# Optimization experiments

Hardware: AMD Instinct MI355X
Metric: run time of the kernel (lower is better)

## Reference

```python
import jax, jax.numpy as jnp
import numpy as np

VOCAB = 32000; DIM = 512; NL = 6; B = 2; L = 1024
DI = 2 * DIM      # d_inner (expand=2)
DS = 16           # d_state
DC = 4            # d_conv
DR = DIM // 16    # dt_rank = ceil(512/16) = 32


def setup_inputs() -> dict:
    key = jax.random.key(0)
    ks = jax.random.split(key, 10)
    s = 0.02
    tokens = jax.random.randint(ks[0], (B, L), 0, VOCAB)
    pos_emb = jax.random.normal(ks[1], (1, L, DIM)) * s
    embed = jax.random.normal(ks[2], (VOCAB, DIM)) * s
    lm_w = jax.random.normal(ks[3], (VOCAB, DIM)) * s
    lm_b = jnp.zeros((VOCAB,), jnp.float32)
    in_proj_w = jax.random.normal(ks[4], (NL, 2 * DI, DIM)) * s
    conv_w = jax.random.normal(ks[5], (NL, DI, DC)) * s
    conv_b = jnp.zeros((NL, DI), jnp.float32)
    x_proj_w = jax.random.normal(ks[6], (NL, DR + 2 * DS, DI)) * s
    dt_proj_w = jax.random.normal(ks[7], (NL, DI, DR)) * s
    dt_proj_b = jnp.broadcast_to(jnp.log(jnp.expm1(jnp.float32(0.01))), (NL, DI)).astype(jnp.float32)
    A_log = jnp.log(jnp.broadcast_to(jnp.arange(1, DS + 1, dtype=jnp.float32), (NL, DI, DS)))
    Dp = jnp.ones((NL, DI), jnp.float32)
    out_w = jax.random.normal(ks[8], (NL, DIM, DI)) * s
    ln_g = jnp.ones((NL, DIM), jnp.float32)
    ln_b = jnp.zeros((NL, DIM), jnp.float32)
    return dict(tokens=tokens, pos_emb=pos_emb, embed=embed, lm_w=lm_w, lm_b=lm_b,
                in_proj_w=in_proj_w, conv_w=conv_w, conv_b=conv_b, x_proj_w=x_proj_w,
                dt_proj_w=dt_proj_w, dt_proj_b=dt_proj_b, A_log=A_log, Dp=Dp,
                out_w=out_w, ln_g=ln_g, ln_b=ln_b)


def silu(x):
    return x * jax.nn.sigmoid(x)


def layernorm(x, g, b, eps=1e-5):
    mu = jnp.mean(x, -1, keepdims=True)
    var = jnp.var(x, -1, keepdims=True)
    return (x - mu) * jax.lax.rsqrt(var + eps) * g + b


def causal_dwconv(x, w, b):
    # x: (B,L,DI), w: (DI,DC) depthwise, left-pad causal
    xp = jnp.pad(x, ((0, 0), (DC - 1, 0), (0, 0)))
    y = b
    for k in range(DC):
        y = y + w[:, k] * xp[:, k:k + x.shape[1], :]
    return y


def selective_scan(u, dt, A, Bm, Cm, Dp):
    # u,dt: (B,L,DI); A: (DI,DS); Bm,Cm: (B,L,DS)
    dA = jnp.exp(dt[..., None] * A)                       # (B,L,DI,DS)
    dBu = dt[..., None] * Bm[:, :, None, :] * u[..., None]
    h0 = jnp.zeros((u.shape[0], DI, DS), u.dtype)

    def step(h, inp):
        dA_t, dBu_t, C_t = inp
        h = dA_t * h + dBu_t
        y = jnp.einsum('bdn,bn->bd', h, C_t)
        return h, y

    _, ys = jax.lax.scan(step, h0, (dA.transpose(1, 0, 2, 3),
                                    dBu.transpose(1, 0, 2, 3),
                                    Cm.transpose(1, 0, 2)))
    return ys.transpose(1, 0, 2) + u * Dp


def mamba_block(x, in_w, cw, cb, xp_w, dtw, dtb, A_log, Dp, ow):
    xz = jnp.einsum('bld,ed->ble', x, in_w)               # (B,L,2*DI)
    xc, z = jnp.split(xz, 2, axis=-1)
    xc = silu(causal_dwconv(xc, cw, cb))
    x_dbl = jnp.einsum('bld,ed->ble', xc, xp_w)           # (B,L,DR+2*DS)
    dt, Bm, Cm = jnp.split(x_dbl, [DR, DR + DS], axis=-1)
    dt = jax.nn.softplus(jnp.einsum('blr,dr->bld', dt, dtw) + dtb)
    A = -jnp.exp(A_log)
    y = selective_scan(xc, dt, A, Bm, Cm, Dp)
    y = y * silu(z)
    return jnp.einsum('bld,ed->ble', y, ow)


def reference(tokens, pos_emb, embed, lm_w, lm_b, in_proj_w, conv_w, conv_b,
              x_proj_w, dt_proj_w, dt_proj_b, A_log, Dp, out_w, ln_g, ln_b):
    x = embed[tokens] + pos_emb[:, :tokens.shape[1]]
    for i in range(NL):
        res = x
        x = mamba_block(x, in_proj_w[i], conv_w[i], conv_b[i], x_proj_w[i],
                        dt_proj_w[i], dt_proj_b[i], A_log[i], Dp[i], out_w[i])
        x = layernorm(x + res, ln_g[i], ln_b[i])
    return jnp.einsum('bld,vd->blv', x, lm_w) + lm_b
```

## Files before the change

kernel.cpp:

```cpp
#include <hip/hip_runtime.h>
#include <hip/hip_bf16.h>
#include <math.h>

#define BB 2
#define LL 1024
#define DIM 512
#define NL 6
#define DI 1024
#define DS 16
#define DC 4
#define DR 32
#define VOCAB 32000
#define M_ROWS (BB * LL)
#define CCH 64
#define CHLEN (LL / CCH)
#define KSPLIT 8
#define OSPLIT 2

typedef unsigned short u16;
typedef __attribute__((ext_vector_type(8))) short bf16x8;
typedef __attribute__((ext_vector_type(4))) float f32x4;

__device__ __forceinline__ u16 f2bf(float f) {
    unsigned u = __float_as_uint(f);
    u += 0x7FFF + ((u >> 16) & 1);
    return (u16)(u >> 16);
}
__device__ __forceinline__ float bf2f(u16 h) {
    return __uint_as_float(((unsigned)h) << 16);
}
#define SWZ(r, c) ((c) ^ (((r) >> 1) & 3))

__global__ __launch_bounds__(256) void cast_all(const float* __restrict__ lm,
                                                const float* __restrict__ inw,
                                                const float* __restrict__ ow,
                                                const float* __restrict__ xp,
                                                u16* __restrict__ lmb,
                                                u16* __restrict__ inb,
                                                u16* __restrict__ owb_,
                                                u16* __restrict__ xpb) {
    int idx = blockIdx.x * 256 + threadIdx.x;
    const float* src; u16* dst; int off;
    if (idx < 2048000)      { src = lm;  dst = lmb;  off = idx; }
    else if (idx < 2834432) { src = inw; dst = inb;  off = idx - 2048000; }
    else if (idx < 3227648) { src = ow;  dst = owb_; off = idx - 2834432; }
    else                    { src = xp;  dst = xpb;  off = idx - 3227648; }
    float4 v0 = ((const float4*)src)[off * 2];
    float4 v1 = ((const float4*)src)[off * 2 + 1];
    union { u16 h[8]; int4 v; } r;
    r.h[0] = f2bf(v0.x); r.h[1] = f2bf(v0.y); r.h[2] = f2bf(v0.z); r.h[3] = f2bf(v0.w);
    r.h[4] = f2bf(v1.x); r.h[5] = f2bf(v1.y); r.h[6] = f2bf(v1.z); r.h[7] = f2bf(v1.w);
    ((int4*)dst)[off] = r.v;
}

__global__ __launch_bounds__(256) void embed_kernel(const int* __restrict__ tok,
                                                    const float* __restrict__ pos,
                                                    const float* __restrict__ emb,
                                                    float* __restrict__ x,
                                                    u16* __restrict__ xb) {
    int idx = blockIdx.x * 256 + threadIdx.x;
    int d = idx & (DIM - 1);
    int l = (idx >> 9) & (LL - 1);
    int b = idx >> 19;
    int t = tok[b * LL + l];
    float v = emb[(size_t)t * DIM + d] + pos[l * DIM + d];
    x[idx] = v;
    xb[idx] = f2bf(v);
}

__global__ __launch_bounds__(512) void gemm_256(const u16* __restrict__ A,
                                                const u16* __restrict__ W,
                                                float* __restrict__ C,
                                                const float* __restrict__ bias,
                                                int K, int N) {
    __shared__ __align__(16) char smem_raw[98304];
    u16* As = (u16*)smem_raw;
    u16* Ws = (u16*)(smem_raw + 49152);
    float* Cs = (float*)smem_raw;

    const int t = threadIdx.x;
    const int l = t & 63;
    const int w = t >> 6;
    const int wr = w >> 2;
    const int wc = w & 3;

    const int nwg = gridDim.x;
    const int q8 = nwg >> 3, r8 = nwg & 7;
    const int xcd = blockIdx.x & 7, rank = blockIdx.x >> 3;
    const int wgid = (xcd < r8 ? xcd * (q8 + 1) : r8 * (q8 + 1) + (xcd - r8) * q8) + rank;
    const int bm = (wgid & 7) * 256;
    const int bn = (wgid >> 3) * 256;

    f32x4 acc[8][4] = {};
    const int nt = K >> 5;

    auto STAGE = [&](int bufi, int k0) {
#pragma unroll
        for (int p = 0; p < 2; ++p) {
            const int g = p * 512 + t;
            const int row = g >> 2, slot = g & 3;
            __builtin_amdgcn_global_load_lds(
                (const __attribute__((address_space(1))) unsigned int*)
                    (A + (size_t)(bm + row) * K + k0 + SWZ(row, slot) * 8),
                (__attribute__((address_space(3))) unsigned int*)
                    (As + bufi * 8192 + (p * 512 + w * 64) * 8),
                16, 0, 0);
        }
#pragma unroll
        for (int p = 0; p < 2; ++p) {
            const int g = p * 512 + t;
            const int row = g >> 2, slot = g & 3;
            __builtin_amdgcn_global_load_lds(
                (const __attribute__((address_space(1))) unsigned int*)
                    (W + (size_t)(bn + row) * K + k0 + SWZ(row, slot) * 8),
                (__attribute__((address_space(3))) unsigned int*)
                    (Ws + bufi * 8192 + (p * 512 + w * 64) * 8),
                16, 0, 0);
        }
    };
    auto COMPUTE = [&](int bufi) {
        const u16* Ab = As + bufi * 8192;
        const u16* Wb = Ws + bufi * 8192;
        bf16x8 bfr[4];
#pragma unroll
        for (int ni = 0; ni < 4; ++ni) {
            const int wrow = wc * 64 + ni * 16 + (l & 15);
            bfr[ni] = *(const bf16x8*)(Wb + wrow * 32 + SWZ(wrow, l >> 4) * 8);
        }
        __builtin_amdgcn_s_setprio(1);
#pragma unroll
        for (int mi = 0; mi < 8; ++mi) {
            const int arow = wr * 128 + mi * 16 + (l & 15);
            bf16x8 a = *(const bf16x8*)(Ab + arow * 32 + SWZ(arow, l >> 4) * 8);
#pragma unroll
            for (int ni = 0; ni < 4; ++ni)
                acc[mi][ni] = __builtin_amdgcn_mfma_f32_16x16x32_bf16(bfr[ni], a, acc[mi][ni], 0, 0, 0);
        }
        __builtin_amdgcn_s_setprio(0);
    };

    STAGE(0, 0);
    STAGE(1, 32);
    int b0 = 0;
    for (int tt = 0; tt < nt - 2; ++tt) {
        int b2 = b0 + 2; if (b2 >= 3) b2 -= 3;
        STAGE(b2, (tt + 2) << 5);
        asm volatile("s_waitcnt vmcnt(8)\ns_barrier" ::: "memory");
        COMPUTE(b0);
        asm volatile("s_waitcnt lgkmcnt(0)\ns_barrier" ::: "memory");
        ++b0; if (b0 == 3) b0 = 0;
    }
    asm volatile("s_waitcnt vmcnt(4)\ns_barrier" ::: "memory");
    COMPUTE(b0);
    asm volatile("s_waitcnt lgkmcnt(0)\ns_barrier" ::: "memory");
    ++b0; if (b0 == 3) b0 = 0;
    asm volatile("s_waitcnt vmcnt(0)\ns_barrier" ::: "memory");
    COMPUTE(b0);
    asm volatile("s_waitcnt lgkmcnt(0)" ::: "memory");
    __syncthreads();

#pragma unroll
    for (int pass = 0; pass < 4; ++pass) {
        if (wr == (pass >> 1)) {
            const int pm0 = (pass & 1) * 4;
#pragma unroll
            for (int mi2 = 0; mi2 < 4; ++mi2) {
                const int r = mi2 * 16 + (l & 15);
#pragma unroll
                for (int ni = 0; ni < 4; ++ni) {
                    const int c = wc * 64 + ni * 16 + ((l >> 4) << 2);
                    float4 v;
                    v.x = acc[pm0 + mi2][ni][0]; v.y = acc[pm0 + mi2][ni][1];
                    v.z = acc[pm0 + mi2][ni][2]; v.w = acc[pm0 + mi2][ni][3];
                    *(float4*)(Cs + r * 260 + c) = v;
                }
            }
        }
        __syncthreads();
#pragma unroll
        for (int it = 0; it < 8; ++it) {
            const int idx = it * 512 + t;
            const int r = idx >> 6;
            const int c4 = (idx & 63) * 4;
            float4 v = *(float4*)(Cs + r * 260 + c4);
            if (bias != nullptr) {
                float4 b4 = *(const float4*)(bias + bn + c4);
                v.x += b4.x; v.y += b4.y; v.z += b4.z; v.w += b4.w;
            }
            *(float4*)(C + (size_t)(bm + pass * 64 + r) * N + bn + c4) = v;
        }
        __syncthreads();
    }
}

__global__ __launch_bounds__(256) void gemm_n64(const u16* __restrict__ A,
                                                const u16* __restrict__ W,
                                                float* __restrict__ out,
                                                u16* __restrict__ outb,
                                                const float* __restrict__ bias,
                                                int lda, int ldw, int ldc,
                                                int KS, int pstride) {
    __shared__ __align__(16) char smem_raw[36864];
    u16* As = (u16*)smem_raw;
    u16* Ws = (u16*)(smem_raw + 24576);
    float* Cs = (float*)smem_raw;

    const int t = threadIdx.x;
    const int l = t & 63;
    const int w = t >> 6;
    const int gx = gridDim.x, gy = gridDim.y;
    const int nwg = gx * gy * gridDim.z;
    const int fid = (blockIdx.z * gy + blockIdx.y) * gx + blockIdx.x;
    const int q8 = nwg >> 3, r8 = nwg & 7;
    const int xcd = fid & 7, rank = fid >> 3;
    const int wgid = (xcd < r8 ? xcd * (q8 + 1) : r8 * (q8 + 1) + (xcd - r8) * q8) + rank;
    const int kz = wgid % gx;
    const int bm = ((wgid / gx) % gy) * 128;
    const int bnn = (wgid / (gx * gy)) * 64;
    const int wm = w * 32;

    f32x4 acc[2][4] = {};
    const int nt = KS >> 5;
    const int kbeg = kz * KS;

    auto STAGE = [&](int bufi, int k0) {
#pragma unroll
        for (int p = 0; p < 2; ++p) {
            const int i = p * 256 + w * 64 + l;
            const int row = i >> 2;
            const int kq = SWZ(row, i & 3);
            __builtin_amdgcn_global_load_lds(
                (const __attribute__((address_space(1))) unsigned int*)
                    (A + (size_t)(bm + row) * lda + k0 + kq * 8),
                (__attribute__((address_space(3))) unsigned int*)
                    (As + bufi * 4096 + (p * 256 + w * 64) * 8),
                16, 0, 0);
        }
        {
            const int i = w * 64 + l;
            const int row = i >> 2;
            const int kq = SWZ(row, i & 3);
            __builtin_amdgcn_global_load_lds(
                (const __attribute__((address_space(1))) unsigned int*)
                    (W + (size_t)(bnn + row) * ldw + k0 + kq * 8),
                (__attribute__((address_space(3))) unsigned int*)
                    (Ws + bufi * 2048 + (w * 64) * 8),
                16, 0, 0);
        }
    };
    auto COMPUTE = [&](int bufi) {
        const u16* Ab = As + bufi * 4096;
        const u16* Wb = Ws + bufi * 2048;
        bf16x8 bfr[4];
#pragma unroll
        for (int ni = 0; ni < 4; ++ni) {
            const int wr2 = ni * 16 + (l & 15);
            bfr[ni] = *(const bf16x8*)(Wb + wr2 * 32 + SWZ(wr2, l >> 4) * 8);
        }
        __builtin_amdgcn_s_setprio(1);
#pragma unroll
        for (int mi = 0; mi < 2; ++mi) {
            const int ar = wm + mi * 16 + (l & 15);
            bf16x8 a = *(const bf16x8*)(Ab + ar * 32 + SWZ(ar, l >> 4) * 8);
#pragma unroll
            for (int ni = 0; ni < 4; ++ni)
                acc[mi][ni] = __builtin_amdgcn_mfma_f32_16x16x32_bf16(bfr[ni], a, acc[mi][ni], 0, 0, 0);
        }
        __builtin_amdgcn_s_setprio(0);
    };

    STAGE(0, kbeg);
    if (nt == 1) {
        asm volatile("s_waitcnt vmcnt(0)\ns_barrier" ::: "memory");
        COMPUTE(0);
        asm volatile("s_waitcnt lgkmcnt(0)" ::: "memory");
    } else {
        STAGE(1, kbeg + 32);
        int b0 = 0;
        for (int tt = 0; tt < nt - 2; ++tt) {
            int b2 = b0 + 2; if (b2 >= 3) b2 -= 3;
            STAGE(b2, kbeg + ((tt + 2) << 5));
            asm volatile("s_waitcnt vmcnt(6)\ns_barrier" ::: "memory");
            COMPUTE(b0);
            asm volatile("s_waitcnt lgkmcnt(0)\ns_barrier" ::: "memory");
            ++b0; if (b0 == 3) b0 = 0;
        }
        asm volatile("s_waitcnt vmcnt(3)\ns_barrier" ::: "memory");
        COMPUTE(b0);
        asm volatile("s_waitcnt lgkmcnt(0)\ns_barrier" ::: "memory");
        ++b0; if (b0 == 3) b0 = 0;
        asm volatile("s_waitcnt vmcnt(0)\ns_barrier" ::: "memory");
        COMPUTE(b0);
        asm volatile("s_waitcnt lgkmcnt(0)" ::: "memory");
    }

    if (outb != nullptr) {
        u16* opb = outb + (size_t)kz * pstride;
#pragma unroll
        for (int mi = 0; mi < 2; ++mi) {
            const int row = bm + wm + mi * 16 + (l & 15);
#pragma unroll
            for (int ni = 0; ni < 4; ++ni) {
                const int col = bnn + ni * 16 + ((l >> 4) << 2);
                ushort4 v;
                v.x = f2bf(acc[mi][ni][0]); v.y = f2bf(acc[mi][ni][1]);
                v.z = f2bf(acc[mi][ni][2]); v.w = f2bf(acc[mi][ni][3]);
                *(ushort4*)(opb + (size_t)row * ldc + col) = v;
            }
        }
    } else {
        float* op = out + (size_t)kz * pstride;
        __syncthreads();
#pragma unroll
        for (int pass = 0; pass < 2; ++pass) {
            if ((w >> 1) == pass) {
                const int rbase = (w & 1) * 32;
#pragma unroll
                for (int mi = 0; mi < 2; ++mi) {
                    const int r = rbase + mi * 16 + (l & 15);
#pragma unroll
                    for (int ni = 0; ni < 4; ++ni) {
                        const int c = ni * 16 + ((l >> 4) << 2);
                        float4 v;
                        v.x = acc[mi][ni][0]; v.y = acc[mi][ni][1];
                        v.z = acc[mi][ni][2]; v.w = acc[mi][ni][3];
                        *(float4*)(Cs + r * 65 + c) = v;
                    }
                }
            }
            __syncthreads();
#pragma unroll
            for (int it = 0; it < 4; ++it) {
                const int idx = it * 256 + t;
                const int r = idx >> 4;
                const int c4 = (idx & 15) * 4;
                float4 v = *(float4*)(Cs + r * 65 + c4);
                if (bias != nullptr) {
                    float4 b4 = *(const float4*)(bias + bnn + c4);
                    v.x += b4.x; v.y += b4.y; v.z += b4.z; v.w += b4.w;
                }
                *(float4*)(op + (size_t)(bm + pass * 64 + r) * ldc + bnn + c4) = v;
            }
            __syncthreads();
        }
    }
}

__global__ __launch_bounds__(256) void conv_silu(const u16* __restrict__ xzb,
                                                 const float* __restrict__ cw,
                                                 const float* __restrict__ cb,
                                                 u16* __restrict__ xcb) {
    int idx8 = blockIdx.x * 256 + threadIdx.x;
    int c0 = (idx8 & 127) * 8;
    int m = idx8 >> 7;
    int l = m & (LL - 1);

    float acc[8];
    float4 cb0 = *(const float4*)(cb + c0);
    float4 cb1 = *(const float4*)(cb + c0 + 4);
    acc[0] = cb0.x; acc[1] = cb0.y; acc[2] = cb0.z; acc[3] = cb0.w;
    acc[4] = cb1.x; acc[5] = cb1.y; acc[6] = cb1.z; acc[7] = cb1.w;
#pragma unroll
    for (int k = 0; k < DC; ++k) {
        int ll = l + k - (DC - 1);
        if (ll < 0) continue;
        const u16* row = xzb + ((size_t)(m + k - (DC - 1))) * (2 * DI) + c0;
        ushort4 r0 = *(const ushort4*)row;
        ushort4 r1 = *(const ushort4*)(row + 4);
#pragma unroll
        for (int j = 0; j < 4; ++j) {
            acc[j]     += cw[(c0 + j) * DC + k]     * bf2f(((const u16*)&r0)[j]);
            acc[j + 4] += cw[(c0 + j + 4) * DC + k] * bf2f(((const u16*)&r1)[j]);
        }
    }
    ushort4 o0, o1;
#pragma unroll
    for (int j = 0; j < 4; ++j) {
        float v0 = acc[j]     / (1.f + __expf(-acc[j]));
        float v1 = acc[j + 4] / (1.f + __expf(-acc[j + 4]));
        ((u16*)&o0)[j] = f2bf(v0);
        ((u16*)&o1)[j] = f2bf(v1);
    }
    u16* op = xcb + (size_t)idx8 * 8;
    *(ushort4*)op = o0;
    *(ushort4*)(op + 4) = o1;
}

__global__ __launch_bounds__(256) void scan_pass1(const u16* __restrict__ xcb,
                                                  const float* __restrict__ Pf,
                                                  const float* __restrict__ dtw,
                                                  const float* __restrict__ dtb,
                                                  const float* __restrict__ A_log,
                                                  float* __restrict__ S,
                                                  float* __restrict__ Q) {
    __shared__ float xds[CHLEN][64];
    const int t = threadIdx.x;
    const int d = blockIdx.x * 256 + t;
    const int b = blockIdx.y;
    const int c = blockIdx.z;
    const int l0 = c * CHLEN;
    const int m0 = b * LL + l0;

    for (int i = t; i < CHLEN * 64; i += 256) {
        int r = i >> 6, cc = i & 63;
        float s = 0.f;
#pragma unroll
        for (int kz = 0; kz < KSPLIT; ++kz)
            s += Pf[(size_t)kz * (M_ROWS * 64) + (m0 + r) * 64 + cc];
        xds[r][cc] = s;
    }
    __syncthreads();

    float4 wreg[8];
#pragma unroll
    for (int kk = 0; kk < 8; ++kk)
        wreg[kk] = *(const float4*)(dtw + (size_t)d * DR + kk * 4);
    const float dtbv = dtb[d];

    float a[DS];
#pragma unroll
    for (int q = 0; q < 4; ++q) {
        float4 al = *(const float4*)(A_log + d * DS + q * 4);
        a[q * 4 + 0] = -__expf(al.x);
        a[q * 4 + 1] = -__expf(al.y);
        a[q * 4 + 2] = -__expf(al.z);
        a[q * 4 + 3] = -__expf(al.w);
    }
    float Qr[DS];
#pragma unroll
    for (int n = 0; n < DS; ++n) Qr[n] = 0.f;
    float Ssum = 0.f;

    const u16* up = xcb + (size_t)m0 * DI + d;

    for (int l = 0; l < CHLEN; ++l) {
        float dacc = dtbv;
#pragma unroll
        for (int kk = 0; kk < 8; ++kk) {
            float4 xv = *(const float4*)&xds[l][kk * 4];
            dacc += wreg[kk].x * xv.x + wreg[kk].y * xv.y +
                    wreg[kk].z * xv.z + wreg[kk].w * xv.w;
        }
        float dtv = (dacc > 20.f) ? dacc : log1pf(__expf(dacc));
        float uv = bf2f(up[(size_t)l * DI]);
        float wv = dtv * uv;
        Ssum += dtv;
#pragma unroll
        for (int q = 0; q < 4; ++q) {
            float4 Bv = *(const float4*)&xds[l][32 + q * 4];
            float dA0 = __expf(dtv * a[q * 4 + 0]);
            float dA1 = __expf(dtv * a[q * 4 + 1]);
            float dA2 = __expf(dtv * a[q * 4 + 2]);
            float dA3 = __expf(dtv * a[q * 4 + 3]);
            Qr[q * 4 + 0] = dA0 * Qr[q * 4 + 0] + wv * Bv.x;
            Qr[q * 4 + 1] = dA1 * Qr[q * 4 + 1] + wv * Bv.y;
            Qr[q * 4 + 2] = dA2 * Qr[q * 4 + 2] + wv * Bv.z;
            Qr[q * 4 + 3] = dA3 * Qr[q * 4 + 3] + wv * Bv.w;
        }
    }
    S[((size_t)b * CCH + c) * DI + d] = Ssum;
    float* Qp = Q + (((size_t)b * CCH + c) * DI + d) * DS;
#pragma unroll
    for (int q = 0; q < 4; ++q) {
        float4 o;
        o.x = Qr[q * 4 + 0]; o.y = Qr[q * 4 + 1];
        o.z = Qr[q * 4 + 2]; o.w = Qr[q * 4 + 3];
        *(float4*)(Qp + q * 4) = o;
    }
}

__global__ __launch_bounds__(64) void scan_pass2(const float* __restrict__ A_log,
                                                 const float* __restrict__ S,
                                                 float* __restrict__ Q) {
    const int idx = blockIdx.x * 64 + threadIdx.x;
    const int b = idx >> 14;
    const int dn = idx & 16383;
    const int d = dn >> 4;
    const float a = -__expf(A_log[dn]);
    float h = 0.f;
    for (int c = 0; c < CCH; ++c) {
        const size_t soff = ((size_t)b * CCH + c) * DI + d;
        const size_t qoff = ((size_t)b * CCH + c) * (size_t)(DI * DS) + dn;
        float P = __expf(a * S[soff]);
        float qv = Q[qoff];
        Q[qoff] = h;
        h = P * h + qv;
    }
}

__global__ __launch_bounds__(256) void scan_pass3(const u16* __restrict__ xcb,
                                                  const float* __restrict__ Pf,
                                                  const float* __restrict__ dtw,
                                                  const float* __restrict__ dtb,
                                                  const u16* __restrict__ xzb,
                                                  const float* __restrict__ A_log,
                                                  const float* __restrict__ Dpp,
                                                  const float* __restrict__ Q,
                                                  u16* __restrict__ y) {
    __shared__ float xds[CHLEN][64];
    const int t = threadIdx.x;
    const int d = blockIdx.x * 256 + t;
    const int b = blockIdx.y;
    const int c = blockIdx.z;
    const int l0 = c * CHLEN;
    const int m0 = b * LL + l0;

    for (int i = t; i < CHLEN * 64; i += 256) {
        int r = i >> 6, cc = i & 63;
        float s = 0.f;
#pragma unroll
        for (int kz = 0; kz < KSPLIT; ++kz)
            s += Pf[(size_t)kz * (M_ROWS * 64) + (m0 + r) * 64 + cc];
        xds[r][cc] = s;
    }
    __syncthreads();

    float4 wreg[8];
#pragma unroll
    for (int kk = 0; kk < 8; ++kk)
        wreg[kk] = *(const float4*)(dtw + (size_t)d * DR + kk * 4);
    const float dtbv = dtb[d];

    float a[DS];
#pragma unroll
    for (int q = 0; q < 4; ++q) {
        float4 al = *(const float4*)(A_log + d * DS + q * 4);
        a[q * 4 + 0] = -__expf(al.x);
        a[q * 4 + 1] = -__expf(al.y);
        a[q * 4 + 2] = -__expf(al.z);
        a[q * 4 + 3] = -__expf(al.w);
    }
    float h[DS];
    const float* Qp = Q + (((size_t)b * CCH + c) * DI + d) * DS;
#pragma unroll
    for (int q = 0; q < 4; ++q) {
        float4 hv = *(const float4*)(Qp + q * 4);
        h[q * 4 + 0] = hv.x; h[q * 4 + 1] = hv.y;
        h[q * 4 + 2] = hv.z; h[q * 4 + 3] = hv.w;
    }
    const float dp = Dpp[d];

    const u16* up = xcb + (size_t)m0 * DI + d;
    const u16* zp = xzb + (size_t)m0 * (2 * DI) + DI + d;
    u16* yp = y + (size_t)m0 * DI + d;

    for (int l = 0; l < CHLEN; ++l) {
        float dacc = dtbv;
#pragma unroll
        for (int kk = 0; kk < 8; ++kk) {
            float4 xv = *(const float4*)&xds[l][kk * 4];
            dacc += wreg[kk].x * xv.x + wreg[kk].y * xv.y +
                    wreg[kk].z * xv.z + wreg[kk].w * xv.w;
        }
        float dtv = (dacc > 20.f) ? dacc : log1pf(__expf(dacc));
        float uv = bf2f(up[(size_t)l * DI]);
        float wv = dtv * uv;
        float p = 0.f;
#pragma unroll
        for (int q = 0; q < 4; ++q) {
            float4 Bv = *(const float4*)&xds[l][32 + q * 4];
            float4 Cv = *(const float4*)&xds[l][48 + q * 4];
            float dA0 = __expf(dtv * a[q * 4 + 0]);
            float dA1 = __expf(dtv * a[q * 4 + 1]);
            float dA2 = __expf(dtv * a[q * 4 + 2]);
            float dA3 = __expf(dtv * a[q * 4 + 3]);
            h[q * 4 + 0] = dA0 * h[q * 4 + 0] + wv * Bv.x;
            h[q * 4 + 1] = dA1 * h[q * 4 + 1] + wv * Bv.y;
            h[q * 4 + 2] = dA2 * h[q * 4 + 2] + wv * Bv.z;
            h[q * 4 + 3] = dA3 * h[q * 4 + 3] + wv * Bv.w;
            p += h[q * 4 + 0] * Cv.x + h[q * 4 + 1] * Cv.y +
                 h[q * 4 + 2] * Cv.z + h[q * 4 + 3] * Cv.w;
        }
        float zv = bf2f(zp[(size_t)l * (2 * DI)]);
        float g = zv / (1.f + __expf(-zv));
        yp[(size_t)l * DI] = f2bf((p + uv * dp) * g);
    }
}

__global__ __launch_bounds__(256) void add_ln(const float* __restrict__ opart,
                                              float* __restrict__ x,
                                              const float* __restrict__ g,
                                              const float* __restrict__ b,
                                              u16* __restrict__ xb) {
    const int PS = M_ROWS * DIM;
    int m = blockIdx.x;
    int t = threadIdx.x;
    const float* xr = x + (size_t)m * DIM;
    float v0 = xr[t];
    float v1 = xr[t + 256];
#pragma unroll
    for (int kz = 0; kz < OSPLIT; ++kz) {
        const float* op = opart + (size_t)kz * PS + (size_t)m * DIM;
        v0 += op[t];
        v1 += op[t + 256];
    }
    float s = v0 + v1;
    float ss = v0 * v0 + v1 * v1;
#pragma unroll
    for (int off = 32; off > 0; off >>= 1) {
        s += __shfl_down(s, off, 64);
        ss += __shfl_down(ss, off, 64);
    }
    __shared__ float sb[4], ssb[4];
    int w = t >> 6;
    if ((t & 63) == 0) { sb[w] = s; ssb[w] = ss; }
    __syncthreads();
    float stot = sb[0] + sb[1] + sb[2] + sb[3];
    float sstot = ssb[0] + ssb[1] + ssb[2] + ssb[3];
    float mean = stot * (1.f / DIM);
    float var = sstot * (1.f / DIM) - mean * mean;
    float rs = rsqrtf(var + 1e-5f);
    float* xw = x + (size_t)m * DIM;
    float o0 = (v0 - mean) * rs * g[t] + b[t];
    float o1 = (v1 - mean) * rs * g[t + 256] + b[t + 256];
    xw[t] = o0;
    xw[t + 256] = o1;
    xb[(size_t)m * DIM + t] = f2bf(o0);
    xb[(size_t)m * DIM + t + 256] = f2bf(o1);
}

extern "C" void kernel_launch(void* const* d_in, const int* in_sizes, int n_in,
                              void* d_out, int out_size, void* d_ws, size_t ws_size,
                              hipStream_t stream) {
    const int*   tokens = (const int*)d_in[0];
    const float* pos    = (const float*)d_in[1];
    const float* emb    = (const float*)d_in[2];
    const float* lm_w   = (const float*)d_in[3];
    const float* lm_b   = (const float*)d_in[4];
    const float* in_w   = (const float*)d_in[5];
    const float* cw     = (const float*)d_in[6];
    const float* cb     = (const float*)d_in[7];
    const float* xpw    = (const float*)d_in[8];
    const float* dtw    = (const float*)d_in[9];
    const float* dtb    = (const float*)d_in[10];
    const float* A_log  = (const float*)d_in[11];
    const float* Dpp    = (const float*)d_in[12];
    const float* ow     = (const float*)d_in[13];
    const float* lng    = (const float*)d_in[14];
    const float* lnb    = (const float*)d_in[15];
    float* out = (float*)d_out;

    float* ws = (float*)d_ws;
    float* x    = ws;
    float* S    = x + 1048576;
    float* Qb   = S + 131072;
    float* Pf   = Qb + 2097152;
    float* Pf2  = Pf + 1048576;
    u16* xzb    = (u16*)(Pf2 + 2097152);
    u16* xb     = xzb + 4194304;
    u16* yb     = xb + 1048576;
    u16* xcb    = yb + 2097152;
    u16* lm_wb  = xcb + 2097152;
    u16* in_wb  = lm_wb + 16384000;
    u16* owb    = in_wb + 6291456;
    u16* xpwb   = owb + 3145728;

    cast_all<<<12800, 256, 0, stream>>>(lm_w, in_w, ow, xpw,
                                        lm_wb, in_wb, owb, xpwb);

    embed_kernel<<<M_ROWS * DIM / 256, 256, 0, stream>>>(tokens, pos, emb, x, xb);

    for (int i = 0; i < NL; ++i) {
        gemm_n64<<<dim3(1, M_ROWS / 128, 2048 / 64), 256, 0, stream>>>(
            xb, in_wb + (size_t)i * 2048 * 512, nullptr, xzb, nullptr,
            512, 512, 2048, 512, 0);
        conv_silu<<<M_ROWS * DI / 8 / 256, 256, 0, stream>>>(
            xzb, cw + (size_t)i * DI * DC, cb + (size_t)i * DI, xcb);
        gemm_n64<<<dim3(KSPLIT, M_ROWS / 128, 1), 256, 0, stream>>>(
            xcb, xpwb + (size_t)i * 64 * 1024, Pf, nullptr, nullptr,
            1024, 1024, 64, 1024 / KSPLIT, M_ROWS * 64);
        scan_pass1<<<dim3(DI / 256, BB, CCH), 256, 0, stream>>>(
            xcb, Pf, dtw + (size_t)i * DI * DR, dtb + (size_t)i * DI,
            A_log + (size_t)i * DI * DS, S, Qb);
        scan_pass2<<<(BB * DI * DS) / 64, 64, 0, stream>>>(
            A_log + (size_t)i * DI * DS, S, Qb);
        scan_pass3<<<dim3(DI / 256, BB, CCH), 256, 0, stream>>>(
            xcb, Pf, dtw + (size_t)i * DI * DR, dtb + (size_t)i * DI, xzb,
            A_log + (size_t)i * DI * DS, Dpp + (size_t)i * DI, Qb, yb);
        gemm_n64<<<dim3(OSPLIT, M_ROWS / 128, 512 / 64), 256, 0, stream>>>(
            yb, owb + (size_t)i * 512 * 1024, Pf2, nullptr, nullptr,
            1024, 1024, 512, 1024 / OSPLIT, M_ROWS * 512);
        add_ln<<<M_ROWS, 256, 0, stream>>>(
            Pf2, x, lng + (size_t)i * DIM, lnb + (size_t)i * DIM, xb);
    }

    gemm_256<<<(M_ROWS / 256) * (VOCAB / 256), 512, 0, stream>>>(
        xb, lm_wb, out, lm_b, 512, VOCAB);
}
```

Baseline: 793.9 us.

## Fuse three scan passes into one cooperative kernel with grid syncs

Merges the chunked selective-scan passes (per-chunk local scan, cross-chunk carry propagation, final output pass) into a single cooperative kernel separated by grid-wide syncs. Each block keeps its dt, A and xds state in registers and shared memory across phases. This removes two kernel launches per layer and the recomputation of the projection reduction and dt weights in the third pass. In exchange it adds grid barrier overhead, requires all 512 blocks to be co-resident, and the carry phase now runs 256-thread blocks in a sequential loop over chunks.

New measurement: 1.671 ms. 2.11x slower.

```diff
diff --git a/kernel.cpp b/kernel.cpp
--- a/kernel.cpp
+++ b/kernel.cpp
@@ -1,6 +1,9 @@
 #include <hip/hip_runtime.h>
 #include <hip/hip_bf16.h>
+#include <hip/hip_cooperative_groups.h>
 #include <math.h>
+
+namespace cg = cooperative_groups;
 
 #define BB 2
 #define LL 1024
@@ -386,13 +389,16 @@
     *(ushort4*)(op + 4) = o1;
 }
 
-__global__ __launch_bounds__(256) void scan_pass1(const u16* __restrict__ xcb,
-                                                  const float* __restrict__ Pf,
-                                                  const float* __restrict__ dtw,
-                                                  const float* __restrict__ dtb,
-                                                  const float* __restrict__ A_log,
-                                                  float* __restrict__ S,
-                                                  float* __restrict__ Q) {
+__global__ __launch_bounds__(256) void scan_coop(const u16* __restrict__ xcb,
+                                                 const float* __restrict__ Pf,
+                                                 const float* __restrict__ dtw,
+                                                 const float* __restrict__ dtb,
+                                                 const u16* __restrict__ xzb,
+                                                 const float* __restrict__ A_log,
+                                                 const float* __restrict__ Dpp,
+                                                 float* S,
+                                                 float* Q,
+                                                 u16* __restrict__ y) {
     __shared__ float xds[CHLEN][64];
     const int t = threadIdx.x;
     const int d = blockIdx.x * 256 + t;
@@ -426,11 +432,11 @@
         a[q * 4 + 2] = -__expf(al.z);
         a[q * 4 + 3] = -__expf(al.w);
     }
+
     float Qr[DS];
 #pragma unroll
     for (int n = 0; n < DS; ++n) Qr[n] = 0.f;
     float Ssum = 0.f;
-
     const u16* up = xcb + (size_t)m0 * DI + d;
 
     for (int l = 0; l < CHLEN; ++l) {
@@ -459,88 +465,52 @@
         }
     }
     S[((size_t)b * CCH + c) * DI + d] = Ssum;
-    float* Qp = Q + (((size_t)b * CCH + c) * DI + d) * DS;
-#pragma unroll
-    for (int q = 0; q < 4; ++q) {
-        float4 o;
-        o.x = Qr[q * 4 + 0]; o.y = Qr[q * 4 + 1];
-        o.z = Qr[q * 4 + 2]; o.w = Qr[q * 4 + 3];
-        *(float4*)(Qp + q * 4) = o;
-    }
-}
-
-__global__ __launch_bounds__(64) void scan_pass2(const float* __restrict__ A_log,
-                                                 const float* __restrict__ S,
-                                                 float* __restrict__ Q) {
-    const int idx = blockIdx.x * 64 + threadIdx.x;
-    const int b = idx >> 14;
-    const int dn = idx & 16383;
-    const int d = dn >> 4;
-    const float a = -__expf(A_log[dn]);
-    float h = 0.f;
-    for (int c = 0; c < CCH; ++c) {
-        const size_t soff = ((size_t)b * CCH + c) * DI + d;
-        const size_t qoff = ((size_t)b * CCH + c) * (size_t)(DI * DS) + dn;
-        float P = __expf(a * S[soff]);
-        float qv = Q[qoff];
-        Q[qoff] = h;
-        h = P * h + qv;
-    }
-}
-
-__global__ __launch_bounds__(256) void scan_pass3(const u16* __restrict__ xcb,
-                                                  const float* __restrict__ Pf,
-                                                  const float* __restrict__ dtw,
-                                                  const float* __restrict__ dtb,
-                                                  const u16* __restrict__ xzb,
-                                                  const float* __restrict__ A_log,
-                                                  const float* __restrict__ Dpp,
-                                                  const float* __restrict__ Q,
-                                                  u16* __restrict__ y) {
-    __shared__ float xds[CHLEN][64];
-    const int t = threadIdx.x;
-    const int d = blockIdx.x * 256 + t;
-    const int b = blockIdx.y;
-    const int c = blockIdx.z;
-    const int l0 = c * CHLEN;
-    const int m0 = b * LL + l0;
-
-    for (int i = t; i < CHLEN * 64; i += 256) {
-        int r = i >> 6, cc = i & 63;
-        float s = 0.f;
-#pragma unroll
-        for (int kz = 0; kz < KSPLIT; ++kz)
-            s += Pf[(size_t)kz * (M_ROWS * 64) + (m0 + r) * 64 + cc];
-        xds[r][cc] = s;
-    }
-    __syncthreads();
-
-    float4 wreg[8];
-#pragma unroll
-    for (int kk = 0; kk < 8; ++kk)
-        wreg[kk] = *(const float4*)(dtw + (size_t)d * DR + kk * 4);
-    const float dtbv = dtb[d];
-
-    float a[DS];
-#pragma unroll
-    for (int q = 0; q < 4; ++q) {
-        float4 al = *(const float4*)(A_log + d * DS + q * 4);
-        a[q * 4 + 0] = -__expf(al.x);
-        a[q * 4 + 1] = -__expf(al.y);
-        a[q * 4 + 2] = -__expf(al.z);
-        a[q * 4 + 3] = -__expf(al.w);
-    }
+    {
+        float* Qp = Q + (((size_t)b * CCH + c) * DI + d) * DS;
+#pragma unroll
+        for (int q = 0; q < 4; ++q) {
+            float4 o;
+            o.x = Qr[q * 4 + 0]; o.y = Qr[q * 4 + 1];
+            o.z = Qr[q * 4 + 2]; o.w = Qr[q * 4 + 3];
+            *(float4*)(Qp + q * 4) = o;
+        }
+    }
+
+    cg::this_grid().sync();
+
+    {
+        const int fid = (blockIdx.z * gridDim.y + blockIdx.y) * gridDim.x + blockIdx.x;
+        const int gtid = fid * 256 + t;
+        if (gtid < BB * DI * DS) {
+            const int b2 = gtid >> 14;
+            const int dn = gtid & 16383;
+            const int d2 = dn >> 4;
+            const float a2 = -__expf(A_log[dn]);
+            float h2 = 0.f;
+            for (int c2 = 0; c2 < CCH; ++c2) {
+                const size_t soff = ((size_t)b2 * CCH + c2) * DI + d2;
+                const size_t qoff = ((size_t)b2 * CCH + c2) * (size_t)(DI * DS) + dn;
+                float P = __expf(a2 * S[soff]);
+                float qv = Q[qoff];
+                Q[qoff] = h2;
+                h2 = P * h2 + qv;
+            }
+        }
+    }
+
+    cg::this_grid().sync();
+
     float h[DS];
-    const float* Qp = Q + (((size_t)b * CCH + c) * DI + d) * DS;
-#pragma unroll
-    for (int q = 0; q < 4; ++q) {
-        float4 hv = *(const float4*)(Qp + q * 4);
-        h[q * 4 + 0] = hv.x; h[q * 4 + 1] = hv.y;
-        h[q * 4 + 2] = hv.z; h[q * 4 + 3] = hv.w;
+    {
+        const float* Qp = Q + (((size_t)b * CCH + c) * DI + d) * DS;
+#pragma unroll
+        for (int q = 0; q < 4; ++q) {
+            float4 hv = *(const float4*)(Qp + q * 4);
+            h[q * 4 + 0] = hv.x; h[q * 4 + 1] = hv.y;
+            h[q * 4 + 2] = hv.z; h[q * 4 + 3] = hv.w;
+        }
     }
     const float dp = Dpp[d];
-
-    const u16* up = xcb + (size_t)m0 * DI + d;
     const u16* zp = xzb + (size_t)m0 * (2 * DI) + DI + d;
     u16* yp = y + (size_t)m0 * DI + d;
 
@@ -669,14 +639,25 @@
         gemm_n64<<<dim3(KSPLIT, M_ROWS / 128, 1), 256, 0, stream>>>(
             xcb, xpwb + (size_t)i * 64 * 1024, Pf, nullptr, nullptr,
             1024, 1024, 64, 1024 / KSPLIT, M_ROWS * 64);
-        scan_pass1<<<dim3(DI / 256, BB, CCH), 256, 0, stream>>>(
-            xcb, Pf, dtw + (size_t)i * DI * DR, dtb + (size_t)i * DI,
-            A_log + (size_t)i * DI * DS, S, Qb);
-        scan_pass2<<<(BB * DI * DS) / 64, 64, 0, stream>>>(
-            A_log + (size_t)i * DI * DS, S, Qb);
-        scan_pass3<<<dim3(DI / 256, BB, CCH), 256, 0, stream>>>(
-            xcb, Pf, dtw + (size_t)i * DI * DR, dtb + (size_t)i * DI, xzb,
-            A_log + (size_t)i * DI * DS, Dpp + (size_t)i * DI, Qb, yb);
+        {
+            const u16* xcb_a = xcb;
+            const float* Pf_a = Pf;
+            const float* dtw_a = dtw + (size_t)i * DI * DR;
+            const float* dtb_a = dtb + (size_t)i * DI;
+            const u16* xzb_a = xzb;
+            const float* Alog_a = A_log + (size_t)i * DI * DS;
+            const float* Dpp_a = Dpp + (size_t)i * DI;
+            float* S_a = S;
+            float* Q_a = Qb;
+            u16* y_a = yb;
+            void* kargs[] = {(void*)&xcb_a, (void*)&Pf_a, (void*)&dtw_a,
+                             (void*)&dtb_a, (void*)&xzb_a, (void*)&Alog_a,
+                             (void*)&Dpp_a, (void*)&S_a, (void*)&Q_a,
+                             (void*)&y_a};
+            hipLaunchCooperativeKernel((const void*)scan_coop,
+                                       dim3(DI / 256, BB, CCH), dim3(256),
+                                       kargs, 0, stream);
+        }
         gemm_n64<<<dim3(OSPLIT, M_ROWS / 128, 512 / 64), 256, 0, stream>>>(
             yb, owb + (size_t)i * 512 * 1024, Pf2, nullptr, nullptr,
             1024, 1024, 512, 1024 / OSPLIT, M_ROWS * 512);
```
